# Optimization experiments

Hardware: AMD Instinct MI355X
Metric: run time of the kernel (lower is better)

Reference implementation:

```python
import jax, jax.numpy as jnp
import numpy as np

B = 65536
IN_F = 512
OUT_F = 256
NUM_GROUPS = 8
EPS = 1e-5


def setup_inputs() -> dict:
    key = jax.random.key(0)
    ks = jax.random.split(key, 6)
    return {
        "x": jax.random.normal(ks[0], (B, IN_F), dtype=jnp.float32),
        "weight": jax.random.normal(ks[1], (OUT_F, IN_F), dtype=jnp.float32) * 0.05,
        "bias_linear": jax.random.normal(ks[2], (OUT_F,), dtype=jnp.float32) * 0.05,
        "weight_gn": jax.random.normal(ks[3], (OUT_F,), dtype=jnp.float32),
        "bias_gn": jax.random.normal(ks[4], (OUT_F,), dtype=jnp.float32),
        "bias": jax.random.normal(ks[5], (1, OUT_F, 1, 1), dtype=jnp.float32),
    }


def reference(x, weight, bias_linear, weight_gn, bias_gn, bias):
    # Linear: (B, IN_F) @ (IN_F, OUT_F) + bias -> (B, OUT_F)
    h = jnp.einsum("bi,oi->bo", x, weight) + bias_linear
    # GroupNorm over channel dim (dim=1) with NUM_GROUPS groups
    g = h.reshape(B, NUM_GROUPS, OUT_F // NUM_GROUPS)
    mean = jnp.mean(g, axis=2, keepdims=True)
    var = jnp.mean(jnp.square(g - mean), axis=2, keepdims=True)
    gn = ((g - mean) * jax.lax.rsqrt(var + EPS)).reshape(B, OUT_F)
    gn = gn * weight_gn + bias_gn
    # Min over channels, keepdim -> (B, 1)
    min_vals = jnp.min(gn, axis=1, keepdims=True)
    # torch broadcasting: (B,1) + (1,256,1,1) -> (1,256,B,1)
    result = min_vals + bias
    return result
```

## Files before the change

### kernel.cpp

```cpp
#include <hip/hip_runtime.h>
#include <hip/hip_bf16.h>

#define B_ROWS 65536
#define K_DIM  512
#define N_DIM  256
#define EPS    1e-5f
#define MTILE  32
#define NBLK   256
#define STRIDE 520

using short8  = __attribute__((ext_vector_type(8))) short;
using floatx4 = __attribute__((ext_vector_type(4))) float;

__device__ __forceinline__ unsigned short f2bf(float f) {
    unsigned u = __builtin_bit_cast(unsigned, f);
    u += 0x7FFFu + ((u >> 16) & 1u);
    return (unsigned short)(u >> 16);
}

__global__ __launch_bounds__(64) void pack_w(const float* __restrict__ W,
                                             unsigned short* __restrict__ P) {
    int b    = blockIdx.x;
    int nt   = b >> 4, kk = b & 15;
    int lane = threadIdx.x;
    int l15  = lane & 15, quad = lane >> 4;
    const float* src = W + (size_t)(nt * 16 + l15) * K_DIM + kk * 32 + quad * 8;
    short8 v;
#pragma unroll
    for (int j = 0; j < 8; ++j) v[j] = (short)f2bf(src[j]);
    *(short8*)(P + ((size_t)(nt * 16 + kk) * 64 + lane) * 8) = v;
}

__global__ __launch_bounds__(512, 2) void fused_persistent(
    const float* __restrict__ X, const unsigned short* __restrict__ P,
    const float* __restrict__ bias_lin, const float* __restrict__ wgn,
    const float* __restrict__ bgn, const float* __restrict__ bias,
    float* __restrict__ out)
{
    __shared__ unsigned short Ash[MTILE * STRIDE];
    __shared__ float sm_min[8][MTILE];
    __shared__ float m_sh[MTILE];

    const int tid  = threadIdx.x;
    const int wave = tid >> 6, lane = tid & 63;
    const int l15  = lane & 15, quad = lane >> 4;

    short8 bfr[2][16];
#pragma unroll
    for (int ct = 0; ct < 2; ++ct)
#pragma unroll
        for (int kkg = 0; kkg < 16; ++kkg) {
            int nt = 2 * wave + ct;
            bfr[ct][kkg] = *(const short8*)(P + (((size_t)nt * 16 + kkg) * 64 + lane) * 8);
        }

    float bl[2], wg[2], bg[2];
#pragma unroll
    for (int ct = 0; ct < 2; ++ct) {
        int col = wave * 32 + ct * 16 + l15;
        bl[ct] = bias_lin[col]; wg[ct] = wgn[col]; bg[ct] = bgn[col];
    }
    float bias_r[4];
#pragma unroll
    for (int pass = 0; pass < 4; ++pass) bias_r[pass] = bias[pass * 64 + (tid >> 3)];

    const int r0 = tid >> 7;
    const int c4 = (tid & 127) * 4;

    const int tiles = B_ROWS / MTILE;
    int t = blockIdx.x;

    float4 xq[8];
#pragma unroll
    for (int p = 0; p < 8; ++p)
        xq[p] = *(const float4*)(X + (size_t)(t * MTILE + r0 + 4 * p) * K_DIM + c4);

    for (; t < tiles; t += NBLK) {
#pragma unroll
        for (int p = 0; p < 8; ++p) {
            ushort4 h;
            h.x = f2bf(xq[p].x); h.y = f2bf(xq[p].y);
            h.z = f2bf(xq[p].z); h.w = f2bf(xq[p].w);
            *(ushort4*)(&Ash[(r0 + 4 * p) * STRIDE + c4]) = h;
        }
        __syncthreads();

        int tn = t + NBLK;
        if (tn < tiles) {
#pragma unroll
            for (int p = 0; p < 8; ++p)
                xq[p] = *(const float4*)(X + (size_t)(tn * MTILE + r0 + 4 * p) * K_DIM + c4);
        }

        floatx4 acc[2][2] = {};
#pragma unroll
        for (int kk = 0; kk < 16; ++kk) {
            short8 a0 = *(const short8*)&Ash[(l15)      * STRIDE + kk * 32 + quad * 8];
            short8 a1 = *(const short8*)&Ash[(16 + l15) * STRIDE + kk * 32 + quad * 8];
            acc[0][0] = __builtin_amdgcn_mfma_f32_16x16x32_bf16(a0, bfr[0][kk], acc[0][0], 0, 0, 0);
            acc[0][1] = __builtin_amdgcn_mfma_f32_16x16x32_bf16(a0, bfr[1][kk], acc[0][1], 0, 0, 0);
            acc[1][0] = __builtin_amdgcn_mfma_f32_16x16x32_bf16(a1, bfr[0][kk], acc[1][0], 0, 0, 0);
            acc[1][1] = __builtin_amdgcn_mfma_f32_16x16x32_bf16(a1, bfr[1][kk], acc[1][1], 0, 0, 0);
        }

#pragma unroll
        for (int rt = 0; rt < 2; ++rt) {
#pragma unroll
            for (int reg = 0; reg < 4; ++reg) {
                float va = acc[rt][0][reg] + bl[0];
                float vb = acc[rt][1][reg] + bl[1];
                float s = va + vb, ss = va * va + vb * vb;
#pragma unroll
                for (int m = 1; m < 16; m <<= 1) {
                    s  += __shfl_xor(s, m);
                    ss += __shfl_xor(ss, m);
                }
                float mean = s * (1.0f / 32.0f);
                float var  = ss * (1.0f / 32.0f) - mean * mean;
                float inv  = rsqrtf(var + EPS);
                float ga = (va - mean) * inv * wg[0] + bg[0];
                float gb = (vb - mean) * inv * wg[1] + bg[1];
                float mn = fminf(ga, gb);
#pragma unroll
                for (int m = 1; m < 16; m <<= 1) mn = fminf(mn, __shfl_xor(mn, m));
                if (l15 == 0) sm_min[wave][rt * 16 + quad * 4 + reg] = mn;
            }
        }
        __syncthreads();
        if (tid < MTILE) {
            float m0 = sm_min[0][tid];
#pragma unroll
            for (int w = 1; w < 8; ++w) m0 = fminf(m0, sm_min[w][tid]);
            m_sh[tid] = m0;
        }
        __syncthreads();

        float4 mv = *(const float4*)&m_sh[(tid & 7) * 4];
#pragma unroll
        for (int pass = 0; pass < 4; ++pass) {
            int c = pass * 64 + (tid >> 3);
            float bc = bias_r[pass];
            float4 o;
            o.x = mv.x + bc; o.y = mv.y + bc; o.z = mv.z + bc; o.w = mv.w + bc;
            *(float4*)(out + (size_t)c * B_ROWS + t * MTILE + (tid & 7) * 4) = o;
        }
    }
}

extern "C" void kernel_launch(void* const* d_in, const int* in_sizes, int n_in,
                              void* d_out, int out_size, void* d_ws, size_t ws_size,
                              hipStream_t stream) {
    const float* x    = (const float*)d_in[0];
    const float* w    = (const float*)d_in[1];
    const float* bl   = (const float*)d_in[2];
    const float* wg   = (const float*)d_in[3];
    const float* bg   = (const float*)d_in[4];
    const float* bias = (const float*)d_in[5];

    unsigned short* P = (unsigned short*)d_ws;
    float* out = (float*)d_out;

    hipLaunchKernelGGL(pack_w, dim3(256), dim3(64), 0, stream, w, P);
    hipLaunchKernelGGL(fused_persistent, dim3(NBLK), dim3(512), 0, stream,
                       x, P, bl, wg, bg, bias, out);
}
```

Measured before the change: 236.3 us.

## Use 1024-thread blocks and stage GEMM results through swizzled LDS for GroupNorm

Doubles the block to 16 waves, each owning a single 16-column tile of the weight, which halves the MFMA and register work per wave. The accumulators are written into an XOR-swizzled shared buffer that aliases the X tile. GroupNorm statistics and the channel min are then computed by 4-thread teams per row and group, replacing long 16-lane shuffle chains. This adds an extra barrier and an LDS round trip per tile. It also asks for 4 blocks of 1024 threads per CU in launch bounds, which may cap registers tightly.

```diff
diff --git a/kernel.cpp b/kernel.cpp
--- a/kernel.cpp
+++ b/kernel.cpp
@@ -3,11 +3,12 @@
 
 #define B_ROWS 65536
 #define K_DIM  512
-#define N_DIM  256
 #define EPS    1e-5f
 #define MTILE  32
 #define NBLK   256
-#define STRIDE 520
+#define NTILES (B_ROWS / MTILE)
+#define XSTR   520
+#define HSTR   264
 
 using short8  = __attribute__((ext_vector_type(8))) short;
 using floatx4 = __attribute__((ext_vector_type(4))) float;
@@ -31,118 +32,141 @@
     *(short8*)(P + ((size_t)(nt * 16 + kk) * 64 + lane) * 8) = v;
 }
 
-__global__ __launch_bounds__(512, 2) void fused_persistent(
+__global__ __launch_bounds__(1024, 4) void fused(
     const float* __restrict__ X, const unsigned short* __restrict__ P,
     const float* __restrict__ bias_lin, const float* __restrict__ wgn,
     const float* __restrict__ bgn, const float* __restrict__ bias,
     float* __restrict__ out)
 {
-    __shared__ unsigned short Ash[MTILE * STRIDE];
-    __shared__ float sm_min[8][MTILE];
+    __shared__ union {
+        unsigned short x[MTILE * XSTR];
+        float          h[MTILE * HSTR];
+    } S;
+    __shared__ float wg_sh[256], bg_sh[256], bias_sh[256];
+    __shared__ float Msh[MTILE * 8];
     __shared__ float m_sh[MTILE];
 
     const int tid  = threadIdx.x;
     const int wave = tid >> 6, lane = tid & 63;
     const int l15  = lane & 15, quad = lane >> 4;
 
-    short8 bfr[2][16];
+    if (tid < 256) { wg_sh[tid] = wgn[tid]; bg_sh[tid] = bgn[tid]; bias_sh[tid] = bias[tid]; }
+
+    short8 bfr[16];
 #pragma unroll
-    for (int ct = 0; ct < 2; ++ct)
+    for (int kk = 0; kk < 16; ++kk)
+        bfr[kk] = *(const short8*)(P + (((size_t)wave * 16 + kk) * 64 + lane) * 8);
+
+    const float bl = bias_lin[wave * 16 + l15];
+
+    const int sr = tid >> 5;
+    const int sc = tid & 31;
+
+    const int pr   = (tid >> 2) & 31;
+    const int pg   = tid >> 7;
+    const int part = tid & 3;
+    const int c0   = pg * 8 + part * 2;
+    const int r7   = pr & 7;
+
+    __syncthreads();
+    const float bias_r0 = bias_sh[tid >> 3];
+    const float bias_r1 = bias_sh[(tid >> 3) + 128];
+
+    int t = blockIdx.x;
+    float4 xq[4];
 #pragma unroll
-        for (int kkg = 0; kkg < 16; ++kkg) {
-            int nt = 2 * wave + ct;
-            bfr[ct][kkg] = *(const short8*)(P + (((size_t)nt * 16 + kkg) * 64 + lane) * 8);
-        }
+    for (int p = 0; p < 4; ++p)
+        xq[p] = *(const float4*)(X + (size_t)(t * MTILE + sr) * K_DIM + (sc + 32 * p) * 4);
 
-    float bl[2], wg[2], bg[2];
+    for (; t < NTILES; t += NBLK) {
 #pragma unroll
-    for (int ct = 0; ct < 2; ++ct) {
-        int col = wave * 32 + ct * 16 + l15;
-        bl[ct] = bias_lin[col]; wg[ct] = wgn[col]; bg[ct] = bgn[col];
-    }
-    float bias_r[4];
-#pragma unroll
-    for (int pass = 0; pass < 4; ++pass) bias_r[pass] = bias[pass * 64 + (tid >> 3)];
-
-    const int r0 = tid >> 7;
-    const int c4 = (tid & 127) * 4;
-
-    const int tiles = B_ROWS / MTILE;
-    int t = blockIdx.x;
-
-    float4 xq[8];
-#pragma unroll
-    for (int p = 0; p < 8; ++p)
-        xq[p] = *(const float4*)(X + (size_t)(t * MTILE + r0 + 4 * p) * K_DIM + c4);
-
-    for (; t < tiles; t += NBLK) {
-#pragma unroll
-        for (int p = 0; p < 8; ++p) {
-            ushort4 h;
-            h.x = f2bf(xq[p].x); h.y = f2bf(xq[p].y);
-            h.z = f2bf(xq[p].z); h.w = f2bf(xq[p].w);
-            *(ushort4*)(&Ash[(r0 + 4 * p) * STRIDE + c4]) = h;
+        for (int p = 0; p < 4; ++p) {
+            ushort4 hx;
+            hx.x = f2bf(xq[p].x); hx.y = f2bf(xq[p].y);
+            hx.z = f2bf(xq[p].z); hx.w = f2bf(xq[p].w);
+            *(ushort4*)(&S.x[sr * XSTR + (sc + 32 * p) * 4]) = hx;
         }
         __syncthreads();
 
         int tn = t + NBLK;
-        if (tn < tiles) {
+        if (tn < NTILES) {
 #pragma unroll
-            for (int p = 0; p < 8; ++p)
-                xq[p] = *(const float4*)(X + (size_t)(tn * MTILE + r0 + 4 * p) * K_DIM + c4);
+            for (int p = 0; p < 4; ++p)
+                xq[p] = *(const float4*)(X + (size_t)(tn * MTILE + sr) * K_DIM + (sc + 32 * p) * 4);
         }
 
-        floatx4 acc[2][2] = {};
+        floatx4 acc0 = {0.f, 0.f, 0.f, 0.f};
+        floatx4 acc1 = {0.f, 0.f, 0.f, 0.f};
 #pragma unroll
         for (int kk = 0; kk < 16; ++kk) {
-            short8 a0 = *(const short8*)&Ash[(l15)      * STRIDE + kk * 32 + quad * 8];
-            short8 a1 = *(const short8*)&Ash[(16 + l15) * STRIDE + kk * 32 + quad * 8];
-            acc[0][0] = __builtin_amdgcn_mfma_f32_16x16x32_bf16(a0, bfr[0][kk], acc[0][0], 0, 0, 0);
-            acc[0][1] = __builtin_amdgcn_mfma_f32_16x16x32_bf16(a0, bfr[1][kk], acc[0][1], 0, 0, 0);
-            acc[1][0] = __builtin_amdgcn_mfma_f32_16x16x32_bf16(a1, bfr[0][kk], acc[1][0], 0, 0, 0);
-            acc[1][1] = __builtin_amdgcn_mfma_f32_16x16x32_bf16(a1, bfr[1][kk], acc[1][1], 0, 0, 0);
+            short8 a0 = *(const short8*)&S.x[l15 * XSTR + kk * 32 + quad * 8];
+            short8 a1 = *(const short8*)&S.x[(16 + l15) * XSTR + kk * 32 + quad * 8];
+            acc0 = __builtin_amdgcn_mfma_f32_16x16x32_bf16(a0, bfr[kk], acc0, 0, 0, 0);
+            acc1 = __builtin_amdgcn_mfma_f32_16x16x32_bf16(a1, bfr[kk], acc1, 0, 0, 0);
         }
+        __syncthreads();
 
+        {
+            const int chq = (wave * 16 + l15) >> 2, chl = l15 & 3;
 #pragma unroll
-        for (int rt = 0; rt < 2; ++rt) {
+            for (int rt = 0; rt < 2; ++rt) {
+                floatx4 a = rt ? acc1 : acc0;
 #pragma unroll
-            for (int reg = 0; reg < 4; ++reg) {
-                float va = acc[rt][0][reg] + bl[0];
-                float vb = acc[rt][1][reg] + bl[1];
-                float s = va + vb, ss = va * va + vb * vb;
-#pragma unroll
-                for (int m = 1; m < 16; m <<= 1) {
-                    s  += __shfl_xor(s, m);
-                    ss += __shfl_xor(ss, m);
+                for (int reg = 0; reg < 4; ++reg) {
+                    int row = rt * 16 + quad * 4 + reg;
+                    S.h[row * HSTR + ((chq ^ (row & 7)) << 2) + chl] = a[reg] + bl;
                 }
-                float mean = s * (1.0f / 32.0f);
-                float var  = ss * (1.0f / 32.0f) - mean * mean;
-                float inv  = rsqrtf(var + EPS);
-                float ga = (va - mean) * inv * wg[0] + bg[0];
-                float gb = (vb - mean) * inv * wg[1] + bg[1];
-                float mn = fminf(ga, gb);
-#pragma unroll
-                for (int m = 1; m < 16; m <<= 1) mn = fminf(mn, __shfl_xor(mn, m));
-                if (l15 == 0) sm_min[wave][rt * 16 + quad * 4 + reg] = mn;
             }
         }
         __syncthreads();
+
+        {
+            float4 v0 = *(const float4*)&S.h[pr * HSTR + (((c0)     ^ r7) << 2)];
+            float4 v1 = *(const float4*)&S.h[pr * HSTR + (((c0 + 1) ^ r7) << 2)];
+            float s  = (v0.x + v0.y) + (v0.z + v0.w) + (v1.x + v1.y) + (v1.z + v1.w);
+            float ss = (v0.x*v0.x + v0.y*v0.y) + (v0.z*v0.z + v0.w*v0.w)
+                     + (v1.x*v1.x + v1.y*v1.y) + (v1.z*v1.z + v1.w*v1.w);
+            s  += __shfl_xor(s, 1);  ss += __shfl_xor(ss, 1);
+            s  += __shfl_xor(s, 2);  ss += __shfl_xor(ss, 2);
+            float mean = s * (1.0f / 32.0f);
+            float var  = ss * (1.0f / 32.0f) - mean * mean;
+            float inv  = rsqrtf(var + EPS);
+            float4 w0 = *(const float4*)&wg_sh[c0 * 4];
+            float4 w1 = *(const float4*)&wg_sh[c0 * 4 + 4];
+            float4 b0 = *(const float4*)&bg_sh[c0 * 4];
+            float4 b1 = *(const float4*)&bg_sh[c0 * 4 + 4];
+            float mn = fminf(
+                fminf(fminf((v0.x - mean) * inv * w0.x + b0.x,
+                            (v0.y - mean) * inv * w0.y + b0.y),
+                      fminf((v0.z - mean) * inv * w0.z + b0.z,
+                            (v0.w - mean) * inv * w0.w + b0.w)),
+                fminf(fminf((v1.x - mean) * inv * w1.x + b1.x,
+                            (v1.y - mean) * inv * w1.y + b1.y),
+                      fminf((v1.z - mean) * inv * w1.z + b1.z,
+                            (v1.w - mean) * inv * w1.w + b1.w)));
+            mn = fminf(mn, __shfl_xor(mn, 1));
+            mn = fminf(mn, __shfl_xor(mn, 2));
+            if (part == 0) Msh[pr * 8 + pg] = mn;
+        }
+        __syncthreads();
         if (tid < MTILE) {
-            float m0 = sm_min[0][tid];
+            float m0 = Msh[tid * 8 + 0];
 #pragma unroll
-            for (int w = 1; w < 8; ++w) m0 = fminf(m0, sm_min[w][tid]);
+            for (int g = 1; g < 8; ++g) m0 = fminf(m0, Msh[tid * 8 + g]);
             m_sh[tid] = m0;
         }
         __syncthreads();
 
-        float4 mv = *(const float4*)&m_sh[(tid & 7) * 4];
-#pragma unroll
-        for (int pass = 0; pass < 4; ++pass) {
-            int c = pass * 64 + (tid >> 3);
-            float bc = bias_r[pass];
-            float4 o;
-            o.x = mv.x + bc; o.y = mv.y + bc; o.z = mv.z + bc; o.w = mv.w + bc;
-            *(float4*)(out + (size_t)c * B_ROWS + t * MTILE + (tid & 7) * 4) = o;
+        {
+            float4 mv = *(const float4*)&m_sh[(tid & 7) * 4];
+            int c = tid >> 3;
+            float4 o0, o1;
+            o0.x = mv.x + bias_r0; o0.y = mv.y + bias_r0;
+            o0.z = mv.z + bias_r0; o0.w = mv.w + bias_r0;
+            o1.x = mv.x + bias_r1; o1.y = mv.y + bias_r1;
+            o1.z = mv.z + bias_r1; o1.w = mv.w + bias_r1;
+            *(float4*)(out + (size_t)c * B_ROWS + t * MTILE + (tid & 7) * 4) = o0;
+            *(float4*)(out + (size_t)(c + 128) * B_ROWS + t * MTILE + (tid & 7) * 4) = o1;
         }
     }
 }
@@ -161,6 +185,6 @@
     float* out = (float*)d_out;
 
     hipLaunchKernelGGL(pack_w, dim3(256), dim3(64), 0, stream, w, P);
-    hipLaunchKernelGGL(fused_persistent, dim3(NBLK), dim3(512), 0, stream,
+    hipLaunchKernelGGL(fused, dim3(NBLK), dim3(1024), 0, stream,
                        x, P, bl, wg, bg, bias, out);
 }
```

Result: slower. 258.2 us (+9.3%).
